# Kernel tuning notes

Hardware: AMD Instinct MI355X
Metric: run time of the kernel (lower is better)

## Reference

```python
import jax, jax.numpy as jnp
import numpy as np

N_NODES = 100000
N_EDGES = 1600000
IN_NODE = 129
HID = 128
N_LAYERS = 3


def setup_inputs() -> dict:
    key = jax.random.key(0)
    ks = jax.random.split(key, 20)
    gnn_in = IN_NODE - 1
    x = jax.random.normal(ks[0], (N_NODES, IN_NODE), dtype=jnp.float32)
    edge_index = jax.random.randint(ks[1], (2, N_EDGES), 0, N_NODES, dtype=jnp.int64)
    edge_attr = jax.random.uniform(ks[2], (N_EDGES, 1), dtype=jnp.float32)
    # conv layer params: lin (in->hid) per layer, scalar edge mlp per layer
    dims = [gnn_in] + [HID] * N_LAYERS
    conv_W, conv_b, edge_w = [], [], []
    for i in range(N_LAYERS):
        fin = dims[i]
        s = 1.0 / np.sqrt(fin)
        conv_W.append(jax.random.uniform(ks[3 + i], (fin, HID), jnp.float32, -s, s))
        conv_b.append(jax.random.uniform(ks[6 + i], (HID,), jnp.float32, -s, s))
        edge_w.append(jax.random.uniform(ks[9 + i], (1, 1), jnp.float32, -1.0, 1.0))
    h2 = HID // 2
    t_h = IN_NODE // 2
    s1 = 1.0 / np.sqrt(HID + 1)
    s2 = 1.0 / np.sqrt(h2)
    s3 = 1.0 / np.sqrt(IN_NODE)
    s4 = 1.0 / np.sqrt(t_h)
    return {
        "x": x, "edge_index": edge_index, "edge_attr": edge_attr,
        "conv_W": tuple(conv_W), "conv_b": tuple(conv_b), "edge_w": tuple(edge_w),
        "lin1_W": jax.random.uniform(ks[12], (HID + 1, h2), jnp.float32, -s1, s1),
        "lin1_b": jax.random.uniform(ks[13], (h2,), jnp.float32, -s1, s1),
        "lin2_W": jax.random.uniform(ks[14], (h2, 1), jnp.float32, -s2, s2),
        "lin2_b": jax.random.uniform(ks[15], (1,), jnp.float32, -s2, s2),
        "t1_W": jax.random.uniform(ks[16], (IN_NODE, t_h), jnp.float32, -s3, s3),
        "t1_b": jax.random.uniform(ks[17], (t_h,), jnp.float32, -s3, s3),
        "t2_W": jax.random.uniform(ks[18], (t_h, 1), jnp.float32, -s4, s4),
        "t2_b": jax.random.uniform(ks[19], (1,), jnp.float32, -s4, s4),
    }


def reference(x, edge_index, edge_attr, conv_W, conv_b, edge_w,
              lin1_W, lin1_b, lin2_W, lin2_b, t1_W, t1_b, t2_W, t2_b):
    n = x.shape[0]
    # add self loops with edge_attr fill_value = 1.0
    loops = jnp.arange(n, dtype=edge_index.dtype)
    src = jnp.concatenate([edge_index[0], loops])
    tgt = jnp.concatenate([edge_index[1], loops])
    ea = jnp.concatenate([edge_attr, jnp.ones((n, 1), edge_attr.dtype)], axis=0)  # [E+N,1]
    # in-degree for mean aggregation (>=1 because of self loops)
    deg = jax.ops.segment_sum(jnp.ones_like(ea[:, 0]), tgt, num_segments=n)[:, None]
    # treatment head (eval mode: no dropout)
    t = jax.nn.relu(x @ t1_W + t1_b)
    t = jax.nn.sigmoid(t @ t2_W + t2_b)  # [N,1]
    h = x[:, 1:]
    for W, b, w in zip(conv_W, conv_b, edge_w):
        ht = h @ W + b                          # [N,HID]
        gate = jax.nn.sigmoid(ea * w[0, 0])     # [E+N,1]
        msg = gate * ht[src]                    # gather + gate
        agg = jax.ops.segment_sum(msg, tgt, num_segments=n) / deg
        h = jax.nn.relu(agg)
    z = jnp.concatenate([h, t], axis=1)          # [N,HID+1]
    z = jax.nn.relu(z @ lin1_W + lin1_b)
    out = jax.nn.sigmoid(z @ lin2_W + lin2_b)[:, 0]  # [N]
    return out
```

## Files before the change

### kernel.cpp

```cpp
#include <hip/hip_runtime.h>
#include <hip/hip_fp16.h>
#include <math.h>


typedef _Float16 f16x8 __attribute__((ext_vector_type(8)));
typedef float f32x4 __attribute__((ext_vector_type(4)));

#define CNT_STRIDE 32

__device__ __forceinline__ float sigmoidf_(float v) { return 1.f / (1.f + expf(-v)); }

__global__ void sentinel_kernel(float* __restrict__ out, int n, float val) {
  int i = blockIdx.x * 256 + threadIdx.x;
  if (i < n) out[i] = val;
}

__global__ void init_kernel(const int* __restrict__ ei, int* __restrict__ flag,
                            int* __restrict__ counts, int n) {
  int i = blockIdx.x * 256 + threadIdx.x;
  if (i < (n + 1) * CNT_STRIDE) counts[i] = 0;
  if (i == 0) {
    int all0 = 1;
    for (int k = 1; k < 512; k += 2) {
      if (ei[k] != 0) { all0 = 0; break; }
    }
    *flag = all0;
  }
}

__global__ void rank_kernel(const int* __restrict__ ei, int E, int n,
                            const int* __restrict__ flag,
                            int* __restrict__ slot, int* __restrict__ counts) {
  int e = blockIdx.x * blockDim.x + threadIdx.x;
  if (e >= E) return;
  int t;
  if (*flag) {
    t = (int)((const long long*)ei)[(size_t)E + e];
  } else {
    t = ei[(size_t)E + e];
  }
  slot[e] = ((unsigned)t < (unsigned)n) ? atomicAdd(&counts[(size_t)t * CNT_STRIDE], 1) : -1;
}

__global__ void scan1_kernel(const int* __restrict__ counts, int n,
                             int* __restrict__ starts, int* __restrict__ bsums) {
  __shared__ int tmp[256];
  int i = blockIdx.x * 256 + threadIdx.x;
  int v = (i <= n) ? counts[(size_t)i * CNT_STRIDE] : 0;
  tmp[threadIdx.x] = v;
  __syncthreads();
  for (int off = 1; off < 256; off <<= 1) {
    int t = (threadIdx.x >= (unsigned)off) ? tmp[threadIdx.x - off] : 0;
    __syncthreads();
    tmp[threadIdx.x] += t;
    __syncthreads();
  }
  if (i <= n) starts[i] = tmp[threadIdx.x] - v;
  if (threadIdx.x == 255) bsums[blockIdx.x] = tmp[255];
}

__global__ void scan2_kernel(int* __restrict__ bsums, int nb) {
  __shared__ int tmp[512];
  int v = (threadIdx.x < (unsigned)nb) ? bsums[threadIdx.x] : 0;
  tmp[threadIdx.x] = v;
  __syncthreads();
  for (int off = 1; off < 512; off <<= 1) {
    int t = (threadIdx.x >= (unsigned)off) ? tmp[threadIdx.x - off] : 0;
    __syncthreads();
    tmp[threadIdx.x] += t;
    __syncthreads();
  }
  if (threadIdx.x < (unsigned)nb) bsums[threadIdx.x] = tmp[threadIdx.x] - v;
}

__global__ void scatter_kernel(const int* __restrict__ ei, const int* __restrict__ slot,
                               const int* __restrict__ starts,
                               const int* __restrict__ bsums,
                               const float* __restrict__ ea, int E, int n,
                               const int* __restrict__ flag,
                               const float* __restrict__ w0p,
                               const float* __restrict__ w1p,
                               const float* __restrict__ w2p,
                               uint2* __restrict__ csr) {
  float w0 = w0p[0], w1 = w1p[0], w2 = w2p[0];
  int f64 = *flag;
  const long long* e64 = (const long long*)ei;
  int base = blockIdx.x * blockDim.x + threadIdx.x;
  int stride = gridDim.x * blockDim.x;
#pragma unroll
  for (int u = 0; u < 4; u++) {
    int e = base + u * stride;
    if (e < E) {
      int sl = slot[e];
      if (sl >= 0) {
        int s, t;
        if (f64) {
          s = (int)e64[e];
          t = (int)e64[(size_t)E + e];
        } else {
          s = ei[e];
          t = ei[(size_t)E + e];
        }
        int pos = starts[t] + bsums[t >> 8] + sl;
        if ((unsigned)pos < (unsigned)E) {
          float a = ea[e];
          unsigned sn = (unsigned)min(max(s, 0), min(n - 1, 0x1ffff));
          unsigned g0 = (unsigned)__float2uint_rn(sigmoidf_(a * w0) * 32767.f);
          unsigned g1 = (unsigned)__float2uint_rn(sigmoidf_(a * w1) * 32767.f);
          unsigned g2 = (unsigned)__float2uint_rn(sigmoidf_(a * w2) * 32767.f);
          csr[pos] = make_uint2(sn | (g0 << 17), g1 | (g2 << 15));
        }
      }
    }
  }
}

__global__ void slice_kernel(const float* __restrict__ x, _Float16* __restrict__ h,
                             float* __restrict__ x0, int n) {
  int idx = blockIdx.x * blockDim.x + threadIdx.x;
  if (idx < n * 128) {
    int node = idx >> 7;
    int k = idx & 127;
    h[idx] = (_Float16)x[(size_t)node * 129 + 1 + k];
  }
  if (idx < n) x0[idx] = x[(size_t)idx * 129];
}

__global__ __launch_bounds__(256) void head_mfma_kernel(const _Float16* __restrict__ h,
    const float* __restrict__ extra, const float* __restrict__ W1,
    const float* __restrict__ b1, const float* __restrict__ w2,
    const float* __restrict__ b2, float* __restrict__ out, int n,
    int hrow0, int xrow) {
  __shared__ __align__(16) _Float16 sB[4 * 4 * 64 * 8];
  __shared__ float sWx[64], sB1[64], sW2[64];
  for (int idx = threadIdx.x; idx < 8192; idx += 256) {
    int k = idx >> 6, col = idx & 63;
    float w = W1[(size_t)(hrow0 + k) * 64 + col];
    int ks = k >> 5, quad = (k >> 3) & 3, j = k & 7;
    int nt = col >> 4, cl = col & 15;
    sB[(((ks * 4 + nt) * 64) + quad * 16 + cl) * 8 + j] = (_Float16)w;
  }
  if (threadIdx.x < 64) {
    sWx[threadIdx.x] = W1[(size_t)xrow * 64 + threadIdx.x];
    sB1[threadIdx.x] = b1[threadIdx.x];
    sW2[threadIdx.x] = w2[threadIdx.x];
  }
  __syncthreads();
  int wv = threadIdx.x >> 6, lane = threadIdx.x & 63;
  int quad = lane >> 4, l15 = lane & 15;
  int n0 = (blockIdx.x * 4 + wv) * 16;
  if (n0 >= n) return;
  int node_a = min(n0 + l15, n - 1);
  const _Float16* hrow = h + (size_t)node_a * 128 + quad * 8;

  f32x4 acc[4];
#pragma unroll
  for (int t = 0; t < 4; t++) acc[t] = (f32x4){0.f, 0.f, 0.f, 0.f};
  for (int ks = 0; ks < 4; ks++) {
    f16x8 afrag = *(const f16x8*)(hrow + ks * 32);
    const f16x8* bp = (const f16x8*)sB;
#pragma unroll
    for (int t = 0; t < 4; t++) {
      f16x8 bfrag = bp[(ks * 4 + t) * 64 + lane];
      acc[t] = __builtin_amdgcn_mfma_f32_16x16x32_f16(afrag, bfrag, acc[t], 0, 0, 0);
    }
  }
  float b2v = b2[0];
  float xv[4], part[4] = {0.f, 0.f, 0.f, 0.f};
#pragma unroll
  for (int r = 0; r < 4; r++) xv[r] = extra[min(n0 + quad * 4 + r, n - 1)];
#pragma unroll
  for (int t = 0; t < 4; t++) {
    int col = t * 16 + l15;
    float wx = sWx[col], bb = sB1[col], w2v = sW2[col];
#pragma unroll
    for (int r = 0; r < 4; r++) {
      float u = fmaxf(acc[t][r] + xv[r] * wx + bb, 0.f);
      part[r] += u * w2v;
    }
  }
#pragma unroll
  for (int r = 0; r < 4; r++) {
    float p = part[r];
    p += __shfl_xor(p, 1); p += __shfl_xor(p, 2);
    p += __shfl_xor(p, 4); p += __shfl_xor(p, 8);
    int node = n0 + quad * 4 + r;
    if (l15 == 0 && node < n) out[node] = sigmoidf_(p + b2v);
  }
}

__global__ __launch_bounds__(256) void gemm_mfma_kernel(const _Float16* __restrict__ h,
    const float* __restrict__ Wg, const float* __restrict__ b,
    unsigned char* __restrict__ out8, float* __restrict__ scales, int n) {
  __shared__ __align__(16) _Float16 sB[4 * 8 * 64 * 8];
  for (int i = threadIdx.x; i < 4096; i += 256) {
    int k = i >> 5;
    int n4 = (i & 31) * 4;
    float4 w4 = ((const float4*)Wg)[i];
    int ks = k >> 5, quad = (k >> 3) & 3, j = k & 7;
#pragma unroll
    for (int c = 0; c < 4; c++) {
      int col = n4 + c;
      int nt = col >> 4, cl = col & 15;
      sB[(((ks * 8 + nt) * 64) + quad * 16 + cl) * 8 + j] =
          (_Float16)((const float*)&w4)[c];
    }
  }
  __syncthreads();
  int wv = threadIdx.x >> 6, lane = threadIdx.x & 63;
  int quad = lane >> 4, l15 = lane & 15;
  int tiles = (n + 63) >> 6;
  for (int tile = blockIdx.x; tile < tiles; tile += gridDim.x) {
    int n0 = (tile * 4 + wv) * 16;
    if (n0 >= n) continue;
    int node_a = min(n0 + l15, n - 1);
    const _Float16* hrow = h + (size_t)node_a * 128 + quad * 8;

    f32x4 acc[8];
#pragma unroll
    for (int t = 0; t < 8; t++) acc[t] = (f32x4){0.f, 0.f, 0.f, 0.f};

    for (int ks = 0; ks < 4; ks++) {
      f16x8 afrag = *(const f16x8*)(hrow + ks * 32);
      const f16x8* bp = (const f16x8*)(sB + ks * 8 * 64 * 8);
#pragma unroll
      for (int t = 0; t < 8; t++) {
        f16x8 bfrag = bp[t * 64 + lane];
        acc[t] = __builtin_amdgcn_mfma_f32_16x16x32_f16(afrag, bfrag, acc[t], 0, 0, 0);
      }
    }
#pragma unroll
    for (int t = 0; t < 8; t++) {
      float bias = b[t * 16 + l15];
#pragma unroll
      for (int r = 0; r < 4; r++) acc[t][r] += bias;
    }
    float mx[4] = {0.f, 0.f, 0.f, 0.f};
#pragma unroll
    for (int t = 0; t < 8; t++)
#pragma unroll
      for (int r = 0; r < 4; r++) mx[r] = fmaxf(mx[r], fabsf(acc[t][r]));
#pragma unroll
    for (int m = 1; m <= 8; m <<= 1) {
#pragma unroll
      for (int r = 0; r < 4; r++) mx[r] = fmaxf(mx[r], __shfl_xor(mx[r], m));
    }
#pragma unroll
    for (int r = 0; r < 4; r++) {
      int node = n0 + quad * 4 + r;
      if (node >= n) continue;
      float inv = (mx[r] > 0.f) ? 127.f / mx[r] : 0.f;
      if (l15 == 0) scales[node] = mx[r] * (1.f / 127.f);
#pragma unroll
      for (int t = 0; t < 8; t++) {
        int u = (int)rintf(acc[t][r] * inv) + 128;
        u = min(max(u, 0), 255);
        out8[(size_t)node * 128 + t * 16 + l15] = (unsigned char)u;
      }
    }
  }
}

template <int LAYER>
__device__ __forceinline__ float gate_(uint2 r) {
  const float inv = 1.f / 32767.f;
  if (LAYER == 0) return (float)(r.x >> 17) * inv;
  if (LAYER == 1) return (float)(r.y & 0x7fffu) * inv;
  return (float)(r.y >> 15) * inv;
}

#define ACC4(u, g)                                   \
  a0 += (float)((u) & 0xffu) * (g);                  \
  a1 += (float)(((u) >> 8) & 0xffu) * (g);           \
  a2 += (float)(((u) >> 16) & 0xffu) * (g);          \
  a3 += (float)((u) >> 24) * (g);

template <int LAYER>
__global__ __launch_bounds__(256) void agg_kernel(const unsigned char* __restrict__ ht8,
    const float* __restrict__ scales, const uint2* __restrict__ csr,
    const int* __restrict__ starts, const int* __restrict__ bsums,
    const float* __restrict__ wp, __half2* __restrict__ hout, int n) {
  int wv = threadIdx.x >> 6, lane = threadIdx.x & 63;
  int node = blockIdx.x * 4 + wv;
  if (node >= n) return;
  int s = starts[node] + bsums[node >> 8];
  int c = starts[node + 1] + bsums[(node + 1) >> 8] - s;
  float gs = sigmoidf_(wp[0]);
  int sub = lane & 31, p = lane >> 5;
  unsigned sub4 = (unsigned)sub * 4u;

  unsigned su = *(const unsigned*)(ht8 + (unsigned)node * 128u + sub4);
  float gsc = (p == 0) ? gs * scales[node] : 0.f;
  float sgs = gsc;
  float a0 = 0.f, a1 = 0.f, a2 = 0.f, a3 = 0.f;
  ACC4(su, gsc)

  int j = 0;
  for (; j + 8 <= c; j += 8) {
    uint2 r0 = csr[s + j + 0 + p], r1 = csr[s + j + 2 + p];
    uint2 r2 = csr[s + j + 4 + p], r3 = csr[s + j + 6 + p];
    unsigned i0 = r0.x & 0x1ffffu, i1 = r1.x & 0x1ffffu;
    unsigned i2 = r2.x & 0x1ffffu, i3 = r3.x & 0x1ffffu;
    unsigned u0 = *(const unsigned*)(ht8 + i0 * 128u + sub4);
    unsigned u1 = *(const unsigned*)(ht8 + i1 * 128u + sub4);
    unsigned u2 = *(const unsigned*)(ht8 + i2 * 128u + sub4);
    unsigned u3 = *(const unsigned*)(ht8 + i3 * 128u + sub4);
    float g0 = gate_<LAYER>(r0) * scales[i0];
    float g1 = gate_<LAYER>(r1) * scales[i1];
    float g2 = gate_<LAYER>(r2) * scales[i2];
    float g3 = gate_<LAYER>(r3) * scales[i3];
    sgs += g0 + g1 + g2 + g3;
    ACC4(u0, g0) ACC4(u1, g1) ACC4(u2, g2) ACC4(u3, g3)
  }
  for (; j + 2 <= c; j += 2) {
    uint2 r = csr[s + j + p];
    unsigned i0 = r.x & 0x1ffffu;
    unsigned u = *(const unsigned*)(ht8 + i0 * 128u + sub4);
    float g = gate_<LAYER>(r) * scales[i0];
    sgs += g;
    ACC4(u, g)
  }
  if (j < c) {
    uint2 r = csr[s + j];
    unsigned i0 = r.x & 0x1ffffu;
    unsigned u = *(const unsigned*)(ht8 + i0 * 128u + sub4);
    float g = (p == 0) ? gate_<LAYER>(r) * scales[i0] : 0.f;
    sgs += g;
    ACC4(u, g)
  }
  a0 += __shfl_xor(a0, 32); a1 += __shfl_xor(a1, 32);
  a2 += __shfl_xor(a2, 32); a3 += __shfl_xor(a3, 32);
  sgs += __shfl_xor(sgs, 32);
  float corr = 128.f * sgs;
  float inv = 1.f / (float)(c + 1);
  a0 = fmaxf((a0 - corr) * inv, 0.f);
  a1 = fmaxf((a1 - corr) * inv, 0.f);
  a2 = fmaxf((a2 - corr) * inv, 0.f);
  a3 = fmaxf((a3 - corr) * inv, 0.f);
  if (p == 0) {
    __half2 h01 = __floats2half2_rn(a0, a1);
    __half2 h23 = __floats2half2_rn(a2, a3);
    uint2 outw;
    outw.x = *(unsigned*)&h01;
    outw.y = *(unsigned*)&h23;
    *(uint2*)((char*)hout + (size_t)node * 256 + (size_t)sub * 8) = outw;
  }
}

extern "C" void kernel_launch(void* const* d_in, const int* in_sizes, int n_in,
                              void* d_out, int out_size, void* d_ws, size_t ws_size,
                              hipStream_t stream) {
  int ob = (out_size + 255) / 256;

  const float *x, *ea, *l1W, *l1b, *l2W, *l2b, *t1W, *t1b, *t2W, *t2b;
  const float *convW[3], *convb[3], *edgew[3];
  const int* ei;

  if (n_in == 20) {
    x = (const float*)d_in[0]; ei = (const int*)d_in[1]; ea = (const float*)d_in[2];
    for (int l = 0; l < 3; l++) {
      convW[l] = (const float*)d_in[3 + l];
      convb[l] = (const float*)d_in[6 + l];
      edgew[l] = (const float*)d_in[9 + l];
    }
    l1W = (const float*)d_in[12]; l1b = (const float*)d_in[13];
    l2W = (const float*)d_in[14]; l2b = (const float*)d_in[15];
    t1W = (const float*)d_in[16]; t1b = (const float*)d_in[17];
    t2W = (const float*)d_in[18]; t2b = (const float*)d_in[19];
  } else if (n_in == 14) {
    x = (const float*)d_in[0]; ei = (const int*)d_in[1]; ea = (const float*)d_in[2];
    const float* cw = (const float*)d_in[3];
    const float* cb = (const float*)d_in[4];
    const float* ew = (const float*)d_in[5];
    for (int l = 0; l < 3; l++) {
      convW[l] = cw + (size_t)l * 128 * 128;
      convb[l] = cb + (size_t)l * 128;
      edgew[l] = ew + l;
    }
    l1W = (const float*)d_in[6];  l1b = (const float*)d_in[7];
    l2W = (const float*)d_in[8];  l2b = (const float*)d_in[9];
    t1W = (const float*)d_in[10]; t1b = (const float*)d_in[11];
    t2W = (const float*)d_in[12]; t2b = (const float*)d_in[13];
  } else {
    sentinel_kernel<<<ob, 256, 0, stream>>>((float*)d_out, out_size,
                                            900.0f + (float)n_in);
    return;
  }

  int n = in_sizes[0] / 129;
  int E = in_sizes[2];

  char* ws = (char*)d_ws;
  size_t off = 0;
  auto take = [&](size_t bytes) -> void* {
    void* p = ws + off;
    off = (off + bytes + 255) & ~(size_t)255;
    return p;
  };
  size_t csr_bytes = (size_t)E * 8;
  size_t cnt_bytes = ((size_t)n + 1) * CNT_STRIDE * 4;
  int*      flag    = (int*)take(256);
  uint2*    csr     = (uint2*)take(csr_bytes > cnt_bytes ? csr_bytes : cnt_bytes);
  int*      counts  = (int*)csr;
  int*      starts  = (int*)take(((size_t)n + 1) * 4);
  int*      bsums   = (int*)take(512 * 4);
  float*    tbuf    = (float*)take((size_t)n * 4);
  float*    x0buf   = (float*)take((size_t)n * 4);
  int*      slot    = (int*)take((size_t)E * 4);
  _Float16* h16     = (_Float16*)take((size_t)n * 128 * 2);
  unsigned char* ht8 = (unsigned char*)take((size_t)n * 128);
  float*    scales  = (float*)take((size_t)n * 4);

  if (off > ws_size) {
    sentinel_kernel<<<ob, 256, 0, stream>>>((float*)d_out, out_size,
                                            1000.0f + (float)(ws_size >> 20));
    return;
  }

  int eb = (E + 255) / 256;
  int nb1 = (n + 1 + 255) / 256;
  int zb = ((n + 1) * CNT_STRIDE + 255) / 256;

  init_kernel<<<zb, 256, 0, stream>>>(ei, flag, counts, n);
  rank_kernel<<<eb, 256, 0, stream>>>(ei, E, n, flag, slot, counts);
  scan1_kernel<<<nb1, 256, 0, stream>>>(counts, n, starts, bsums);
  scan2_kernel<<<1, 512, 0, stream>>>(bsums, nb1);
  scatter_kernel<<<(eb + 3) / 4, 256, 0, stream>>>(ei, slot, starts, bsums, ea, E, n,
                                                   flag, edgew[0], edgew[1], edgew[2],
                                                   csr);

  int sb = (int)(((size_t)n * 128 + 255) / 256);
  slice_kernel<<<sb, 256, 0, stream>>>(x, h16, x0buf, n);
  head_mfma_kernel<<<(n + 63) / 64, 256, 0, stream>>>(h16, x0buf, t1W, t1b, t2W, t2b,
                                                      tbuf, n, 1, 0);

  int gemm_grid = min((n + 63) / 64, 1024);
  gemm_mfma_kernel<<<gemm_grid, 256, 0, stream>>>(h16, convW[0], convb[0], ht8, scales, n);
  agg_kernel<0><<<(n + 3) / 4, 256, 0, stream>>>(ht8, scales, csr, starts, bsums,
                                                 edgew[0], (__half2*)h16, n);
  gemm_mfma_kernel<<<gemm_grid, 256, 0, stream>>>(h16, convW[1], convb[1], ht8, scales, n);
  agg_kernel<1><<<(n + 3) / 4, 256, 0, stream>>>(ht8, scales, csr, starts, bsums,
                                                 edgew[1], (__half2*)h16, n);
  gemm_mfma_kernel<<<gemm_grid, 256, 0, stream>>>(h16, convW[2], convb[2], ht8, scales, n);
  agg_kernel<2><<<(n + 3) / 4, 256, 0, stream>>>(ht8, scales, csr, starts, bsums,
                                                 edgew[2], (__half2*)h16, n);

  head_mfma_kernel<<<(n + 63) / 64, 256, 0, stream>>>(h16, tbuf, l1W, l1b, l2W, l2b,
                                                      (float*)d_out, n, 0, 128);
}
```

Baseline: 508.6 us.

## Fuse rank with slice and scatter with treatment head; drop padded counters

Merges the edge-ranking kernel with the feature slice/convert kernel, and the CSR scatter kernel with the treatment-head MFMA kernel, using block-index ranges inside one launch. This cuts launches and lets independent work overlap on the GPU. Separately, the per-node degree counters are no longer padded to a 32-int stride, which shrinks zeroing and scan traffic but packs counters densely, so atomics on nearby targets can now contend on the same cache lines. The fused kernels carry the larger shared-memory footprint of the head for all blocks, which may lower occupancy of the scatter part.

Result: no change. 517.7 us (+1.8%).

```diff
diff --git a/kernel.cpp b/kernel.cpp
--- a/kernel.cpp
+++ b/kernel.cpp
@@ -6,8 +6,6 @@
 typedef _Float16 f16x8 __attribute__((ext_vector_type(8)));
 typedef float f32x4 __attribute__((ext_vector_type(4)));
 
-#define CNT_STRIDE 32
-
 __device__ __forceinline__ float sigmoidf_(float v) { return 1.f / (1.f + expf(-v)); }
 
 __global__ void sentinel_kernel(float* __restrict__ out, int n, float val) {
@@ -18,7 +16,7 @@
 __global__ void init_kernel(const int* __restrict__ ei, int* __restrict__ flag,
                             int* __restrict__ counts, int n) {
   int i = blockIdx.x * 256 + threadIdx.x;
-  if (i < (n + 1) * CNT_STRIDE) counts[i] = 0;
+  if (i <= n) counts[i] = 0;
   if (i == 0) {
     int all0 = 1;
     for (int k = 1; k < 512; k += 2) {
@@ -28,25 +26,39 @@
   }
 }
 
-__global__ void rank_kernel(const int* __restrict__ ei, int E, int n,
-                            const int* __restrict__ flag,
-                            int* __restrict__ slot, int* __restrict__ counts) {
-  int e = blockIdx.x * blockDim.x + threadIdx.x;
-  if (e >= E) return;
-  int t;
-  if (*flag) {
-    t = (int)((const long long*)ei)[(size_t)E + e];
+__global__ void rank_slice_kernel(const int* __restrict__ ei, int E, int n,
+                                  const int* __restrict__ flag,
+                                  int* __restrict__ slot, int* __restrict__ counts,
+                                  const float* __restrict__ x,
+                                  _Float16* __restrict__ h,
+                                  float* __restrict__ x0, int eb) {
+  int bid = blockIdx.x;
+  if (bid < eb) {
+    int e = bid * 256 + threadIdx.x;
+    if (e >= E) return;
+    int t;
+    if (*flag) {
+      t = (int)((const long long*)ei)[(size_t)E + e];
+    } else {
+      t = ei[(size_t)E + e];
+    }
+    slot[e] = ((unsigned)t < (unsigned)n) ? atomicAdd(&counts[t], 1) : -1;
   } else {
-    t = ei[(size_t)E + e];
-  }
-  slot[e] = ((unsigned)t < (unsigned)n) ? atomicAdd(&counts[(size_t)t * CNT_STRIDE], 1) : -1;
+    int idx = (bid - eb) * 256 + threadIdx.x;
+    if (idx < n * 128) {
+      int node = idx >> 7;
+      int k = idx & 127;
+      h[idx] = (_Float16)x[(size_t)node * 129 + 1 + k];
+    }
+    if (idx < n) x0[idx] = x[(size_t)idx * 129];
+  }
 }
 
 __global__ void scan1_kernel(const int* __restrict__ counts, int n,
                              int* __restrict__ starts, int* __restrict__ bsums) {
   __shared__ int tmp[256];
   int i = blockIdx.x * 256 + threadIdx.x;
-  int v = (i <= n) ? counts[(size_t)i * CNT_STRIDE] : 0;
+  int v = (i <= n) ? counts[i] : 0;
   tmp[threadIdx.x] = v;
   __syncthreads();
   for (int off = 1; off < 256; off <<= 1) {
@@ -73,57 +85,107 @@
   if (threadIdx.x < (unsigned)nb) bsums[threadIdx.x] = tmp[threadIdx.x] - v;
 }
 
-__global__ void scatter_kernel(const int* __restrict__ ei, const int* __restrict__ slot,
-                               const int* __restrict__ starts,
-                               const int* __restrict__ bsums,
-                               const float* __restrict__ ea, int E, int n,
-                               const int* __restrict__ flag,
-                               const float* __restrict__ w0p,
-                               const float* __restrict__ w1p,
-                               const float* __restrict__ w2p,
-                               uint2* __restrict__ csr) {
-  float w0 = w0p[0], w1 = w1p[0], w2 = w2p[0];
-  int f64 = *flag;
-  const long long* e64 = (const long long*)ei;
-  int base = blockIdx.x * blockDim.x + threadIdx.x;
-  int stride = gridDim.x * blockDim.x;
-#pragma unroll
-  for (int u = 0; u < 4; u++) {
-    int e = base + u * stride;
-    if (e < E) {
-      int sl = slot[e];
-      if (sl >= 0) {
-        int s, t;
-        if (f64) {
-          s = (int)e64[e];
-          t = (int)e64[(size_t)E + e];
-        } else {
-          s = ei[e];
-          t = ei[(size_t)E + e];
-        }
-        int pos = starts[t] + bsums[t >> 8] + sl;
-        if ((unsigned)pos < (unsigned)E) {
-          float a = ea[e];
-          unsigned sn = (unsigned)min(max(s, 0), min(n - 1, 0x1ffff));
-          unsigned g0 = (unsigned)__float2uint_rn(sigmoidf_(a * w0) * 32767.f);
-          unsigned g1 = (unsigned)__float2uint_rn(sigmoidf_(a * w1) * 32767.f);
-          unsigned g2 = (unsigned)__float2uint_rn(sigmoidf_(a * w2) * 32767.f);
-          csr[pos] = make_uint2(sn | (g0 << 17), g1 | (g2 << 15));
+__global__ __launch_bounds__(256) void scatter_head_kernel(
+    const int* __restrict__ ei, const int* __restrict__ slot,
+    const int* __restrict__ starts, const int* __restrict__ bsums,
+    const float* __restrict__ ea, int E, int n, const int* __restrict__ flag,
+    const float* __restrict__ w0p, const float* __restrict__ w1p,
+    const float* __restrict__ w2p, uint2* __restrict__ csr, int sgrid,
+    const _Float16* __restrict__ h, const float* __restrict__ extra,
+    const float* __restrict__ W1, const float* __restrict__ b1,
+    const float* __restrict__ w2, const float* __restrict__ b2,
+    float* __restrict__ out, int hrow0, int xrow) {
+  if (blockIdx.x < (unsigned)sgrid) {
+    float w0 = w0p[0], w1 = w1p[0], w2v_ = w2p[0];
+    int f64 = *flag;
+    const long long* e64 = (const long long*)ei;
+    int base = blockIdx.x * 256 + threadIdx.x;
+    int stride = sgrid * 256;
+#pragma unroll
+    for (int u = 0; u < 4; u++) {
+      int e = base + u * stride;
+      if (e < E) {
+        int sl = slot[e];
+        if (sl >= 0) {
+          int s, t;
+          if (f64) {
+            s = (int)e64[e];
+            t = (int)e64[(size_t)E + e];
+          } else {
+            s = ei[e];
+            t = ei[(size_t)E + e];
+          }
+          int pos = starts[t] + bsums[t >> 8] + sl;
+          if ((unsigned)pos < (unsigned)E) {
+            float a = ea[e];
+            unsigned sn = (unsigned)min(max(s, 0), min(n - 1, 0x1ffff));
+            unsigned g0 = (unsigned)__float2uint_rn(sigmoidf_(a * w0) * 32767.f);
+            unsigned g1 = (unsigned)__float2uint_rn(sigmoidf_(a * w1) * 32767.f);
+            unsigned g2 = (unsigned)__float2uint_rn(sigmoidf_(a * w2v_) * 32767.f);
+            csr[pos] = make_uint2(sn | (g0 << 17), g1 | (g2 << 15));
+          }
         }
       }
     }
-  }
-}
-
-__global__ void slice_kernel(const float* __restrict__ x, _Float16* __restrict__ h,
-                             float* __restrict__ x0, int n) {
-  int idx = blockIdx.x * blockDim.x + threadIdx.x;
-  if (idx < n * 128) {
-    int node = idx >> 7;
-    int k = idx & 127;
-    h[idx] = (_Float16)x[(size_t)node * 129 + 1 + k];
-  }
-  if (idx < n) x0[idx] = x[(size_t)idx * 129];
+  } else {
+    __shared__ __align__(16) _Float16 sB[4 * 4 * 64 * 8];
+    __shared__ float sWx[64], sB1[64], sW2[64];
+    for (int idx = threadIdx.x; idx < 8192; idx += 256) {
+      int k = idx >> 6, col = idx & 63;
+      float w = W1[(size_t)(hrow0 + k) * 64 + col];
+      int ks = k >> 5, quad = (k >> 3) & 3, j = k & 7;
+      int nt = col >> 4, cl = col & 15;
+      sB[(((ks * 4 + nt) * 64) + quad * 16 + cl) * 8 + j] = (_Float16)w;
+    }
+    if (threadIdx.x < 64) {
+      sWx[threadIdx.x] = W1[(size_t)xrow * 64 + threadIdx.x];
+      sB1[threadIdx.x] = b1[threadIdx.x];
+      sW2[threadIdx.x] = w2[threadIdx.x];
+    }
+    __syncthreads();
+    int hbid = blockIdx.x - sgrid;
+    int wv = threadIdx.x >> 6, lane = threadIdx.x & 63;
+    int quad = lane >> 4, l15 = lane & 15;
+    int n0 = (hbid * 4 + wv) * 16;
+    if (n0 >= n) return;
+    int node_a = min(n0 + l15, n - 1);
+    const _Float16* hrow = h + (size_t)node_a * 128 + quad * 8;
+
+    f32x4 acc[4];
+#pragma unroll
+    for (int t = 0; t < 4; t++) acc[t] = (f32x4){0.f, 0.f, 0.f, 0.f};
+    for (int ks = 0; ks < 4; ks++) {
+      f16x8 afrag = *(const f16x8*)(hrow + ks * 32);
+      const f16x8* bp = (const f16x8*)sB;
+#pragma unroll
+      for (int t = 0; t < 4; t++) {
+        f16x8 bfrag = bp[(ks * 4 + t) * 64 + lane];
+        acc[t] = __builtin_amdgcn_mfma_f32_16x16x32_f16(afrag, bfrag, acc[t], 0, 0, 0);
+      }
+    }
+    float b2v = b2[0];
+    float xv[4], part[4] = {0.f, 0.f, 0.f, 0.f};
+#pragma unroll
+    for (int r = 0; r < 4; r++) xv[r] = extra[min(n0 + quad * 4 + r, n - 1)];
+#pragma unroll
+    for (int t = 0; t < 4; t++) {
+      int col = t * 16 + l15;
+      float wx = sWx[col], bb = sB1[col], w2v = sW2[col];
+#pragma unroll
+      for (int r = 0; r < 4; r++) {
+        float u = fmaxf(acc[t][r] + xv[r] * wx + bb, 0.f);
+        part[r] += u * w2v;
+      }
+    }
+#pragma unroll
+    for (int r = 0; r < 4; r++) {
+      float p = part[r];
+      p += __shfl_xor(p, 1); p += __shfl_xor(p, 2);
+      p += __shfl_xor(p, 4); p += __shfl_xor(p, 8);
+      int node = n0 + quad * 4 + r;
+      if (l15 == 0 && node < n) out[node] = sigmoidf_(p + b2v);
+    }
+  }
 }
 
 __global__ __launch_bounds__(256) void head_mfma_kernel(const _Float16* __restrict__ h,
@@ -398,7 +460,7 @@
     return p;
   };
   size_t csr_bytes = (size_t)E * 8;
-  size_t cnt_bytes = ((size_t)n + 1) * CNT_STRIDE * 4;
+  size_t cnt_bytes = ((size_t)n + 1) * 4;
   int*      flag    = (int*)take(256);
   uint2*    csr     = (uint2*)take(csr_bytes > cnt_bytes ? csr_bytes : cnt_bytes);
   int*      counts  = (int*)csr;
@@ -419,20 +481,18 @@
 
   int eb = (E + 255) / 256;
   int nb1 = (n + 1 + 255) / 256;
-  int zb = ((n + 1) * CNT_STRIDE + 255) / 256;
-
-  init_kernel<<<zb, 256, 0, stream>>>(ei, flag, counts, n);
-  rank_kernel<<<eb, 256, 0, stream>>>(ei, E, n, flag, slot, counts);
+  int sb = (int)(((size_t)n * 128 + 255) / 256);
+  int sgrid = (eb + 3) / 4;
+  int hgrid = (n + 63) / 64;
+
+  init_kernel<<<nb1, 256, 0, stream>>>(ei, flag, counts, n);
+  rank_slice_kernel<<<eb + sb, 256, 0, stream>>>(ei, E, n, flag, slot, counts,
+                                                 x, h16, x0buf, eb);
   scan1_kernel<<<nb1, 256, 0, stream>>>(counts, n, starts, bsums);
   scan2_kernel<<<1, 512, 0, stream>>>(bsums, nb1);
-  scatter_kernel<<<(eb + 3) / 4, 256, 0, stream>>>(ei, slot, starts, bsums, ea, E, n,
-                                                   flag, edgew[0], edgew[1], edgew[2],
-                                                   csr);
-
-  int sb = (int)(((size_t)n * 128 + 255) / 256);
-  slice_kernel<<<sb, 256, 0, stream>>>(x, h16, x0buf, n);
-  head_mfma_kernel<<<(n + 63) / 64, 256, 0, stream>>>(h16, x0buf, t1W, t1b, t2W, t2b,
-                                                      tbuf, n, 1, 0);
+  scatter_head_kernel<<<sgrid + hgrid, 256, 0, stream>>>(
+      ei, slot, starts, bsums, ea, E, n, flag, edgew[0], edgew[1], edgew[2],
+      csr, sgrid, h16, x0buf, t1W, t1b, t2W, t2b, tbuf, 1, 0);
 
   int gemm_grid = min((n + 63) / 64, 1024);
   gemm_mfma_kernel<<<gemm_grid, 256, 0, stream>>>(h16, convW[0], convb[0], ht8, scales, n);
```

## Build CSR with two-pass block-local radix sort instead of global atomics

Applied to the files above, without the earlier changes.

Replaces the global per-node atomic counting sort (padded counters, slot array, scatter) with a two-level radix sort. It bins edges by target>>8 using shared-memory histograms per edge block, scans those per bin, and reorders records into bins. A per-bin kernel then does the fine sort by the low byte and writes the CSR and absolute starts. This is meant to remove contended global atomics and the large zero-fill of the padded counters. The aggregation kernel also gets a 16-edge unrolled loop and drops the bsums lookup. In exchange it adds an extra staging buffer, more kernel launches, and a nondeterministic edge order within each node.

New measurement: 483.0 us. 1.05x faster.

```diff
diff --git a/kernel.cpp b/kernel.cpp
--- a/kernel.cpp
+++ b/kernel.cpp
@@ -6,7 +6,7 @@
 typedef _Float16 f16x8 __attribute__((ext_vector_type(8)));
 typedef float f32x4 __attribute__((ext_vector_type(4)));
 
-#define CNT_STRIDE 32
+#define EPB 4096
 
 __device__ __forceinline__ float sigmoidf_(float v) { return 1.f / (1.f + expf(-v)); }
 
@@ -15,11 +15,8 @@
   if (i < n) out[i] = val;
 }
 
-__global__ void init_kernel(const int* __restrict__ ei, int* __restrict__ flag,
-                            int* __restrict__ counts, int n) {
-  int i = blockIdx.x * 256 + threadIdx.x;
-  if (i < (n + 1) * CNT_STRIDE) counts[i] = 0;
-  if (i == 0) {
+__global__ void flag_kernel(const int* __restrict__ ei, int* __restrict__ flag) {
+  if (threadIdx.x == 0 && blockIdx.x == 0) {
     int all0 = 1;
     for (int k = 1; k < 512; k += 2) {
       if (ei[k] != 0) { all0 = 0; break; }
@@ -28,25 +25,115 @@
   }
 }
 
-__global__ void rank_kernel(const int* __restrict__ ei, int E, int n,
-                            const int* __restrict__ flag,
-                            int* __restrict__ slot, int* __restrict__ counts) {
-  int e = blockIdx.x * blockDim.x + threadIdx.x;
-  if (e >= E) return;
-  int t;
-  if (*flag) {
-    t = (int)((const long long*)ei)[(size_t)E + e];
-  } else {
-    t = ei[(size_t)E + e];
-  }
-  slot[e] = ((unsigned)t < (unsigned)n) ? atomicAdd(&counts[(size_t)t * CNT_STRIDE], 1) : -1;
-}
-
-__global__ void scan1_kernel(const int* __restrict__ counts, int n,
-                             int* __restrict__ starts, int* __restrict__ bsums) {
+__global__ __launch_bounds__(256) void hist_kernel(const int* __restrict__ ei,
+    int E, int n, const int* __restrict__ flag, int* __restrict__ histA,
+    int nblocksA, int NB) {
+  __shared__ int hl[512];
+  for (int i = threadIdx.x; i < NB; i += 256) hl[i] = 0;
+  __syncthreads();
+  int f64 = *flag;
+  const long long* e64 = (const long long*)ei;
+  int base = blockIdx.x * EPB;
+  int end = min(base + EPB, E);
+  for (int e = base + threadIdx.x; e < end; e += 256) {
+    int t = f64 ? (int)e64[(size_t)E + e] : ei[(size_t)E + e];
+    if ((unsigned)t < (unsigned)n) atomicAdd(&hl[t >> 8], 1);
+  }
+  __syncthreads();
+  for (int i = threadIdx.x; i < NB; i += 256)
+    histA[(size_t)i * nblocksA + blockIdx.x] = hl[i];
+}
+
+__global__ __launch_bounds__(256) void scanrow_kernel(int* __restrict__ histA,
+    int nblocksA, int* __restrict__ binTotal) {
   __shared__ int tmp[256];
-  int i = blockIdx.x * 256 + threadIdx.x;
-  int v = (i <= n) ? counts[(size_t)i * CNT_STRIDE] : 0;
+  int bin = blockIdx.x;
+  int* row = histA + (size_t)bin * nblocksA;
+  int carry = 0;
+  for (int c0 = 0; c0 < nblocksA; c0 += 256) {
+    int i = c0 + threadIdx.x;
+    int v = (i < nblocksA) ? row[i] : 0;
+    tmp[threadIdx.x] = v;
+    __syncthreads();
+    for (int off = 1; off < 256; off <<= 1) {
+      int t = (threadIdx.x >= (unsigned)off) ? tmp[threadIdx.x - off] : 0;
+      __syncthreads();
+      tmp[threadIdx.x] += t;
+      __syncthreads();
+    }
+    if (i < nblocksA) row[i] = carry + tmp[threadIdx.x] - v;
+    carry += tmp[255];
+    __syncthreads();
+  }
+  if (threadIdx.x == 0) binTotal[bin] = carry;
+}
+
+__global__ void binbase_kernel(const int* __restrict__ binTotal, int NB,
+                               int* __restrict__ binBase, int* __restrict__ starts,
+                               int n) {
+  __shared__ int tmp[512];
+  int v = (threadIdx.x < (unsigned)NB) ? binTotal[threadIdx.x] : 0;
+  tmp[threadIdx.x] = v;
+  __syncthreads();
+  for (int off = 1; off < 512; off <<= 1) {
+    int t = (threadIdx.x >= (unsigned)off) ? tmp[threadIdx.x - off] : 0;
+    __syncthreads();
+    tmp[threadIdx.x] += t;
+    __syncthreads();
+  }
+  if (threadIdx.x < (unsigned)NB) binBase[threadIdx.x] = tmp[threadIdx.x] - v;
+  if (threadIdx.x == (unsigned)(NB - 1)) {
+    binBase[NB] = tmp[threadIdx.x];
+    starts[n] = tmp[threadIdx.x];
+  }
+}
+
+__global__ __launch_bounds__(256) void reorder_kernel(const int* __restrict__ ei,
+    const float* __restrict__ ea, int E, int n, const int* __restrict__ flag,
+    const int* __restrict__ histA, int nblocksA, const int* __restrict__ binBase,
+    const float* __restrict__ w0p, const float* __restrict__ w1p,
+    const float* __restrict__ w2p, uint2* __restrict__ brec,
+    unsigned char* __restrict__ bkey, int NB) {
+  __shared__ int cur[512];
+  for (int i = threadIdx.x; i < NB; i += 256)
+    cur[i] = binBase[i] + histA[(size_t)i * nblocksA + blockIdx.x];
+  __syncthreads();
+  float w0 = w0p[0], w1 = w1p[0], w2 = w2p[0];
+  int f64 = *flag;
+  const long long* e64 = (const long long*)ei;
+  int base = blockIdx.x * EPB;
+  int end = min(base + EPB, E);
+  for (int e = base + threadIdx.x; e < end; e += 256) {
+    int s, t;
+    if (f64) { s = (int)e64[e]; t = (int)e64[(size_t)E + e]; }
+    else     { s = ei[e];       t = ei[(size_t)E + e]; }
+    if ((unsigned)t < (unsigned)n) {
+      int pos = atomicAdd(&cur[t >> 8], 1);
+      float a = ea[e];
+      unsigned sn = (unsigned)min(max(s, 0), min(n - 1, 0x1ffff));
+      unsigned g0 = (unsigned)__float2uint_rn(sigmoidf_(a * w0) * 32767.f);
+      unsigned g1 = (unsigned)__float2uint_rn(sigmoidf_(a * w1) * 32767.f);
+      unsigned g2 = (unsigned)__float2uint_rn(sigmoidf_(a * w2) * 32767.f);
+      brec[pos] = make_uint2(sn | (g0 << 17), g1 | (g2 << 15));
+      bkey[pos] = (unsigned char)(t & 255);
+    }
+  }
+}
+
+__global__ __launch_bounds__(256) void fine_kernel(const uint2* __restrict__ brec,
+    const unsigned char* __restrict__ bkey, const int* __restrict__ binBase,
+    int n, uint2* __restrict__ csr, int* __restrict__ starts) {
+  __shared__ int cnt[256];
+  __shared__ int offs[256];
+  __shared__ int tmp[256];
+  int bin = blockIdx.x;
+  int b0 = binBase[bin], b1 = binBase[bin + 1];
+  cnt[threadIdx.x] = 0;
+  __syncthreads();
+  for (int p = b0 + threadIdx.x; p < b1; p += 256)
+    atomicAdd(&cnt[bkey[p]], 1);
+  __syncthreads();
+  int v = cnt[threadIdx.x];
   tmp[threadIdx.x] = v;
   __syncthreads();
   for (int off = 1; off < 256; off <<= 1) {
@@ -55,63 +142,16 @@
     tmp[threadIdx.x] += t;
     __syncthreads();
   }
-  if (i <= n) starts[i] = tmp[threadIdx.x] - v;
-  if (threadIdx.x == 255) bsums[blockIdx.x] = tmp[255];
-}
-
-__global__ void scan2_kernel(int* __restrict__ bsums, int nb) {
-  __shared__ int tmp[512];
-  int v = (threadIdx.x < (unsigned)nb) ? bsums[threadIdx.x] : 0;
-  tmp[threadIdx.x] = v;
-  __syncthreads();
-  for (int off = 1; off < 512; off <<= 1) {
-    int t = (threadIdx.x >= (unsigned)off) ? tmp[threadIdx.x - off] : 0;
-    __syncthreads();
-    tmp[threadIdx.x] += t;
-    __syncthreads();
-  }
-  if (threadIdx.x < (unsigned)nb) bsums[threadIdx.x] = tmp[threadIdx.x] - v;
-}
-
-__global__ void scatter_kernel(const int* __restrict__ ei, const int* __restrict__ slot,
-                               const int* __restrict__ starts,
-                               const int* __restrict__ bsums,
-                               const float* __restrict__ ea, int E, int n,
-                               const int* __restrict__ flag,
-                               const float* __restrict__ w0p,
-                               const float* __restrict__ w1p,
-                               const float* __restrict__ w2p,
-                               uint2* __restrict__ csr) {
-  float w0 = w0p[0], w1 = w1p[0], w2 = w2p[0];
-  int f64 = *flag;
-  const long long* e64 = (const long long*)ei;
-  int base = blockIdx.x * blockDim.x + threadIdx.x;
-  int stride = gridDim.x * blockDim.x;
-#pragma unroll
-  for (int u = 0; u < 4; u++) {
-    int e = base + u * stride;
-    if (e < E) {
-      int sl = slot[e];
-      if (sl >= 0) {
-        int s, t;
-        if (f64) {
-          s = (int)e64[e];
-          t = (int)e64[(size_t)E + e];
-        } else {
-          s = ei[e];
-          t = ei[(size_t)E + e];
-        }
-        int pos = starts[t] + bsums[t >> 8] + sl;
-        if ((unsigned)pos < (unsigned)E) {
-          float a = ea[e];
-          unsigned sn = (unsigned)min(max(s, 0), min(n - 1, 0x1ffff));
-          unsigned g0 = (unsigned)__float2uint_rn(sigmoidf_(a * w0) * 32767.f);
-          unsigned g1 = (unsigned)__float2uint_rn(sigmoidf_(a * w1) * 32767.f);
-          unsigned g2 = (unsigned)__float2uint_rn(sigmoidf_(a * w2) * 32767.f);
-          csr[pos] = make_uint2(sn | (g0 << 17), g1 | (g2 << 15));
-        }
-      }
-    }
+  offs[threadIdx.x] = tmp[threadIdx.x] - v;
+  int node = bin * 256 + threadIdx.x;
+  if (node < n) starts[node] = b0 + offs[threadIdx.x];
+  __syncthreads();
+  cnt[threadIdx.x] = 0;
+  __syncthreads();
+  for (int p = b0 + threadIdx.x; p < b1; p += 256) {
+    int k = bkey[p];
+    int l = atomicAdd(&cnt[k], 1);
+    csr[b0 + offs[k] + l] = brec[p];
   }
 }
 
@@ -278,13 +318,13 @@
 template <int LAYER>
 __global__ __launch_bounds__(256) void agg_kernel(const unsigned char* __restrict__ ht8,
     const float* __restrict__ scales, const uint2* __restrict__ csr,
-    const int* __restrict__ starts, const int* __restrict__ bsums,
-    const float* __restrict__ wp, __half2* __restrict__ hout, int n) {
+    const int* __restrict__ starts, const float* __restrict__ wp,
+    __half2* __restrict__ hout, int n) {
   int wv = threadIdx.x >> 6, lane = threadIdx.x & 63;
   int node = blockIdx.x * 4 + wv;
   if (node >= n) return;
-  int s = starts[node] + bsums[node >> 8];
-  int c = starts[node + 1] + bsums[(node + 1) >> 8] - s;
+  int s = starts[node];
+  int c = starts[node + 1] - s;
   float gs = sigmoidf_(wp[0]);
   int sub = lane & 31, p = lane >> 5;
   unsigned sub4 = (unsigned)sub * 4u;
@@ -296,6 +336,35 @@
   ACC4(su, gsc)
 
   int j = 0;
+  for (; j + 16 <= c; j += 16) {
+    uint2 r0 = csr[s + j + 0 + p],  r1 = csr[s + j + 2 + p];
+    uint2 r2 = csr[s + j + 4 + p],  r3 = csr[s + j + 6 + p];
+    uint2 r4 = csr[s + j + 8 + p],  r5 = csr[s + j + 10 + p];
+    uint2 r6 = csr[s + j + 12 + p], r7 = csr[s + j + 14 + p];
+    unsigned i0 = r0.x & 0x1ffffu, i1 = r1.x & 0x1ffffu;
+    unsigned i2 = r2.x & 0x1ffffu, i3 = r3.x & 0x1ffffu;
+    unsigned i4 = r4.x & 0x1ffffu, i5 = r5.x & 0x1ffffu;
+    unsigned i6 = r6.x & 0x1ffffu, i7 = r7.x & 0x1ffffu;
+    unsigned u0 = *(const unsigned*)(ht8 + i0 * 128u + sub4);
+    unsigned u1 = *(const unsigned*)(ht8 + i1 * 128u + sub4);
+    unsigned u2 = *(const unsigned*)(ht8 + i2 * 128u + sub4);
+    unsigned u3 = *(const unsigned*)(ht8 + i3 * 128u + sub4);
+    unsigned u4 = *(const unsigned*)(ht8 + i4 * 128u + sub4);
+    unsigned u5 = *(const unsigned*)(ht8 + i5 * 128u + sub4);
+    unsigned u6 = *(const unsigned*)(ht8 + i6 * 128u + sub4);
+    unsigned u7 = *(const unsigned*)(ht8 + i7 * 128u + sub4);
+    float g0 = gate_<LAYER>(r0) * scales[i0];
+    float g1 = gate_<LAYER>(r1) * scales[i1];
+    float g2 = gate_<LAYER>(r2) * scales[i2];
+    float g3 = gate_<LAYER>(r3) * scales[i3];
+    float g4 = gate_<LAYER>(r4) * scales[i4];
+    float g5 = gate_<LAYER>(r5) * scales[i5];
+    float g6 = gate_<LAYER>(r6) * scales[i6];
+    float g7 = gate_<LAYER>(r7) * scales[i7];
+    sgs += g0 + g1 + g2 + g3 + g4 + g5 + g6 + g7;
+    ACC4(u0, g0) ACC4(u1, g1) ACC4(u2, g2) ACC4(u3, g3)
+    ACC4(u4, g4) ACC4(u5, g5) ACC4(u6, g6) ACC4(u7, g7)
+  }
   for (; j + 8 <= c; j += 8) {
     uint2 r0 = csr[s + j + 0 + p], r1 = csr[s + j + 2 + p];
     uint2 r2 = csr[s + j + 4 + p], r3 = csr[s + j + 6 + p];
@@ -390,6 +459,9 @@
   int n = in_sizes[0] / 129;
   int E = in_sizes[2];
 
+  int nblocksA = (E + EPB - 1) / EPB;
+  int NB = (n + 255) >> 8;
+
   char* ws = (char*)d_ws;
   size_t off = 0;
   auto take = [&](size_t bytes) -> void* {
@@ -397,54 +469,53 @@
     off = (off + bytes + 255) & ~(size_t)255;
     return p;
   };
-  size_t csr_bytes = (size_t)E * 8;
-  size_t cnt_bytes = ((size_t)n + 1) * CNT_STRIDE * 4;
   int*      flag    = (int*)take(256);
-  uint2*    csr     = (uint2*)take(csr_bytes > cnt_bytes ? csr_bytes : cnt_bytes);
-  int*      counts  = (int*)csr;
+  int*      histA   = (int*)take((size_t)NB * nblocksA * 4);
+  int*      binTot  = (int*)take((size_t)NB * 4);
+  int*      binBase = (int*)take(((size_t)NB + 1) * 4);
   int*      starts  = (int*)take(((size_t)n + 1) * 4);
-  int*      bsums   = (int*)take(512 * 4);
+  uint2*    brec    = (uint2*)take((size_t)E * 8);
+  unsigned char* bkey = (unsigned char*)take((size_t)E);
+  uint2*    csr     = (uint2*)take((size_t)E * 8);
   float*    tbuf    = (float*)take((size_t)n * 4);
   float*    x0buf   = (float*)take((size_t)n * 4);
-  int*      slot    = (int*)take((size_t)E * 4);
   _Float16* h16     = (_Float16*)take((size_t)n * 128 * 2);
   unsigned char* ht8 = (unsigned char*)take((size_t)n * 128);
   float*    scales  = (float*)take((size_t)n * 4);
 
-  if (off > ws_size) {
+  if (off > ws_size || nblocksA > 1024 || NB > 512) {
     sentinel_kernel<<<ob, 256, 0, stream>>>((float*)d_out, out_size,
                                             1000.0f + (float)(ws_size >> 20));
     return;
   }
 
-  int eb = (E + 255) / 256;
-  int nb1 = (n + 1 + 255) / 256;
-  int zb = ((n + 1) * CNT_STRIDE + 255) / 256;
-
-  init_kernel<<<zb, 256, 0, stream>>>(ei, flag, counts, n);
-  rank_kernel<<<eb, 256, 0, stream>>>(ei, E, n, flag, slot, counts);
-  scan1_kernel<<<nb1, 256, 0, stream>>>(counts, n, starts, bsums);
-  scan2_kernel<<<1, 512, 0, stream>>>(bsums, nb1);
-  scatter_kernel<<<(eb + 3) / 4, 256, 0, stream>>>(ei, slot, starts, bsums, ea, E, n,
-                                                   flag, edgew[0], edgew[1], edgew[2],
-                                                   csr);
-
   int sb = (int)(((size_t)n * 128 + 255) / 256);
+  int hgrid = (n + 63) / 64;
+
+  flag_kernel<<<1, 64, 0, stream>>>(ei, flag);
+  hist_kernel<<<nblocksA, 256, 0, stream>>>(ei, E, n, flag, histA, nblocksA, NB);
+  scanrow_kernel<<<NB, 256, 0, stream>>>(histA, nblocksA, binTot);
+  binbase_kernel<<<1, 512, 0, stream>>>(binTot, NB, binBase, starts, n);
+  reorder_kernel<<<nblocksA, 256, 0, stream>>>(ei, ea, E, n, flag, histA, nblocksA,
+                                               binBase, edgew[0], edgew[1], edgew[2],
+                                               brec, bkey, NB);
+  fine_kernel<<<NB, 256, 0, stream>>>(brec, bkey, binBase, n, csr, starts);
+
   slice_kernel<<<sb, 256, 0, stream>>>(x, h16, x0buf, n);
-  head_mfma_kernel<<<(n + 63) / 64, 256, 0, stream>>>(h16, x0buf, t1W, t1b, t2W, t2b,
-                                                      tbuf, n, 1, 0);
+  head_mfma_kernel<<<hgrid, 256, 0, stream>>>(h16, x0buf, t1W, t1b, t2W, t2b,
+                                              tbuf, n, 1, 0);
 
   int gemm_grid = min((n + 63) / 64, 1024);
   gemm_mfma_kernel<<<gemm_grid, 256, 0, stream>>>(h16, convW[0], convb[0], ht8, scales, n);
-  agg_kernel<0><<<(n + 3) / 4, 256, 0, stream>>>(ht8, scales, csr, starts, bsums,
+  agg_kernel<0><<<(n + 3) / 4, 256, 0, stream>>>(ht8, scales, csr, starts,
                                                  edgew[0], (__half2*)h16, n);
   gemm_mfma_kernel<<<gemm_grid, 256, 0, stream>>>(h16, convW[1], convb[1], ht8, scales, n);
-  agg_kernel<1><<<(n + 3) / 4, 256, 0, stream>>>(ht8, scales, csr, starts, bsums,
+  agg_kernel<1><<<(n + 3) / 4, 256, 0, stream>>>(ht8, scales, csr, starts,
                                                  edgew[1], (__half2*)h16, n);
   gemm_mfma_kernel<<<gemm_grid, 256, 0, stream>>>(h16, convW[2], convb[2], ht8, scales, n);
-  agg_kernel<2><<<(n + 3) / 4, 256, 0, stream>>>(ht8, scales, csr, starts, bsums,
+  agg_kernel<2><<<(n + 3) / 4, 256, 0, stream>>>(ht8, scales, csr, starts,
                                                  edgew[2], (__half2*)h16, n);
 
-  head_mfma_kernel<<<(n + 63) / 64, 256, 0, stream>>>(h16, tbuf, l1W, l1b, l2W, l2b,
-                                                      (float*)d_out, n, 0, 128);
-}
+  head_mfma_kernel<<<hgrid, 256, 0, stream>>>(h16, tbuf, l1W, l1b, l2W, l2b,
+                                              (float*)d_out, n, 0, 128);
+}
```
